# Kernel tuning notes

Hardware: AMD Instinct MI355X
Metric: run time of the kernel (lower is better)

## Reference

```python
import jax, jax.numpy as jnp
import numpy as np

# Group structure (matches init_kwargs)
SIZES = np.array([16]*16 + [32]*32 + [64]*16)          # teacher_embedding_sizes_list
CHOICES = np.array([4]*16 + [8]*32 + [16]*16)          # max_choice_per_embedding
IN_DIM = int(SIZES.sum())                               # 2304
OUT_DIM = int(CHOICES.sum())                            # 576
W_TOTAL = int((SIZES * CHOICES).sum())                  # 25600
BATCH = 16384


def setup_inputs() -> dict:
    key = jax.random.key(0)
    k1, k2 = jax.random.split(key)
    x = jax.random.normal(k1, (BATCH, IN_DIM), dtype=jnp.float32)
    # TruncatedNormal(stddev=0.15) approximated with scaled normal
    weight = jax.random.normal(k2, (W_TOTAL, 1), dtype=jnp.float32) * 0.15
    bias = jnp.zeros((OUT_DIM,), dtype=jnp.float32)
    return {"x": x, "weight": weight, "bias": bias}


def reference(x, weight, bias):
    # Block-diagonal grouped GEMM: per-group slice of x times per-group weight
    # block reshaped to [size_i, choice_i], concatenated along features + bias.
    w_flat = weight[:, 0]
    outs = []
    w_idx = 0
    t_idx = 0
    for size, choice in zip(SIZES.tolist(), CHOICES.tolist()):
        x_slice = x[:, t_idx:t_idx + size]                       # [B, size]
        w_block = w_flat[w_idx:w_idx + size * choice].reshape(size, choice)
        outs.append(x_slice @ w_block)                           # [B, choice]
        w_idx += size * choice
        t_idx += size
    return jnp.concatenate(outs, axis=1) + bias
```

## Files before the change

### kernel.cpp

```cpp
#include <hip/hip_runtime.h>


#define BATCH   16384
#define IN_DIM  2304
#define OUT_DIM 576
#define CHUNKS  36
#define XS_LDW  68

__global__ __launch_bounds__(256) void fused_block_mm(
    const float* __restrict__ x, const float* __restrict__ w,
    const float* __restrict__ bias, float* __restrict__ out)
{
    __shared__ float xs[64 * XS_LDW];
    __shared__ float wd[64 * 16];

    const int tid = threadIdx.x;
    const int bx  = blockIdx.x;
    const int cj  = bx % CHUNKS;
    const int rt  = bx / CHUNKS;
    const int row_base = rt * 64;

    if (cj < 4) {
        const int wbase = cj * 256;
        #pragma unroll
        for (int i = 0; i < 4; ++i) {
            const int e = tid + i * 256, k = e >> 4, c = e & 15, b = k >> 4;
            wd[e] = ((c >> 2) == b)
                  ? w[wbase + b * 64 + ((k & 15) << 2) + (c & 3)] : 0.0f;
        }
    } else if (cj < 20) {
        const int wbase = 1024 + (cj - 4) * 512;
        #pragma unroll
        for (int i = 0; i < 4; ++i) {
            const int e = tid + i * 256, k = e >> 4, c = e & 15, b = k >> 5;
            wd[e] = ((c >> 3) == b)
                  ? w[wbase + b * 256 + ((k & 31) << 3) + (c & 7)] : 0.0f;
        }
    } else {
        const int wbase = 9216 + (cj - 20) * 1024;
        #pragma unroll
        for (int i = 0; i < 4; ++i) {
            const int e = tid + i * 256;
            wd[e] = w[wbase + e];
        }
    }

    const float* __restrict__ xsrc = x + (size_t)row_base * IN_DIM + cj * 64;
    #pragma unroll
    for (int i = 0; i < 4; ++i) {
        const int f = tid + i * 256, r = f >> 4, c = (f & 15) << 2;
        const float4 v = *reinterpret_cast<const float4*>(
            xsrc + (size_t)r * IN_DIM + c);
        *reinterpret_cast<float4*>(&xs[r * XS_LDW + c]) = v;
    }
    __syncthreads();

    const int wv   = __builtin_amdgcn_readfirstlane(tid >> 6);
    const int lane = tid & 63;
    const int ocol = cj * 16 + (wv << 2);

    float4 acc = make_float4(bias[ocol], bias[ocol + 1],
                             bias[ocol + 2], bias[ocol + 3]);

    const int xb = lane * XS_LDW;
    const int wb = wv << 2;
    #pragma unroll
    for (int k4 = 0; k4 < 16; ++k4) {
        const float4 xv = *reinterpret_cast<const float4*>(&xs[xb + (k4 << 2)]);
        const float4 w0 = *reinterpret_cast<const float4*>(&wd[(k4*4+0)*16 + wb]);
        const float4 w1 = *reinterpret_cast<const float4*>(&wd[(k4*4+1)*16 + wb]);
        const float4 w2 = *reinterpret_cast<const float4*>(&wd[(k4*4+2)*16 + wb]);
        const float4 w3 = *reinterpret_cast<const float4*>(&wd[(k4*4+3)*16 + wb]);
        acc.x += xv.x*w0.x + xv.y*w1.x + xv.z*w2.x + xv.w*w3.x;
        acc.y += xv.x*w0.y + xv.y*w1.y + xv.z*w2.y + xv.w*w3.y;
        acc.z += xv.x*w0.z + xv.y*w1.z + xv.z*w2.z + xv.w*w3.z;
        acc.w += xv.x*w0.w + xv.y*w1.w + xv.z*w2.w + xv.w*w3.w;
    }

    float* __restrict__ op = out + (size_t)(row_base + lane) * OUT_DIM + ocol;
    *reinterpret_cast<float4*>(op) = acc;
}

extern "C" void kernel_launch(void* const* d_in, const int* in_sizes, int n_in,
                              void* d_out, int out_size, void* d_ws, size_t ws_size,
                              hipStream_t stream) {
    const float* x    = (const float*)d_in[0];
    const float* w    = (const float*)d_in[1];
    const float* bias = (const float*)d_in[2];
    float* out        = (float*)d_out;

    const int row_tiles = BATCH / 64;
    fused_block_mm<<<dim3(CHUNKS * row_tiles), 256, 0, stream>>>(
        x, w, bias, out);
}
```

Baseline: 228.6 us.

## Give each wave its own 64-row x tile and all 16 output columns

Each block now has 128 threads (two waves) and covers 128 rows. Each wave loads its own 64-row slice of x into a private shared-memory buffer, and each lane computes all 16 output columns of its row. Before, four waves each computed 4 columns over the same 64 rows. This reuses each x element across 16 outputs in registers, needs no barrier after the x load, and halves the grid size, while the shared weight tile is loaded once per 128 rows. The cost is more accumulator registers per thread and fewer threads per block, so there is less parallelism to hide memory latency on what is a bandwidth-bound kernel.

```diff
diff --git a/kernel.cpp b/kernel.cpp
--- a/kernel.cpp
+++ b/kernel.cpp
@@ -7,78 +7,89 @@
 #define CHUNKS  36
 #define XS_LDW  68
 
-__global__ __launch_bounds__(256) void fused_block_mm(
+__global__ __launch_bounds__(128) void fused_block_mm(
     const float* __restrict__ x, const float* __restrict__ w,
     const float* __restrict__ bias, float* __restrict__ out)
 {
-    __shared__ float xs[64 * XS_LDW];
     __shared__ float wd[64 * 16];
+    __shared__ float xs[2][64 * XS_LDW];
 
     const int tid = threadIdx.x;
     const int bx  = blockIdx.x;
     const int cj  = bx % CHUNKS;
     const int rt  = bx / CHUNKS;
-    const int row_base = rt * 64;
 
     if (cj < 4) {
         const int wbase = cj * 256;
         #pragma unroll
-        for (int i = 0; i < 4; ++i) {
-            const int e = tid + i * 256, k = e >> 4, c = e & 15, b = k >> 4;
+        for (int i = 0; i < 8; ++i) {
+            const int e = tid + i * 128, k = e >> 4, c = e & 15, b = k >> 4;
             wd[e] = ((c >> 2) == b)
                   ? w[wbase + b * 64 + ((k & 15) << 2) + (c & 3)] : 0.0f;
         }
     } else if (cj < 20) {
         const int wbase = 1024 + (cj - 4) * 512;
         #pragma unroll
-        for (int i = 0; i < 4; ++i) {
-            const int e = tid + i * 256, k = e >> 4, c = e & 15, b = k >> 5;
+        for (int i = 0; i < 8; ++i) {
+            const int e = tid + i * 128, k = e >> 4, c = e & 15, b = k >> 5;
             wd[e] = ((c >> 3) == b)
                   ? w[wbase + b * 256 + ((k & 31) << 3) + (c & 7)] : 0.0f;
         }
     } else {
         const int wbase = 9216 + (cj - 20) * 1024;
         #pragma unroll
-        for (int i = 0; i < 4; ++i) {
-            const int e = tid + i * 256;
+        for (int i = 0; i < 8; ++i) {
+            const int e = tid + i * 128;
             wd[e] = w[wbase + e];
         }
     }
+    __syncthreads();
 
-    const float* __restrict__ xsrc = x + (size_t)row_base * IN_DIM + cj * 64;
+    const int wv   = tid >> 6;
+    const int lane = tid & 63;
+    float* __restrict__ xsw = xs[wv];
+    const int row0 = rt * 128 + wv * 64;
+
+    const float* __restrict__ xsrc = x + (size_t)row0 * IN_DIM + cj * 64;
     #pragma unroll
-    for (int i = 0; i < 4; ++i) {
-        const int f = tid + i * 256, r = f >> 4, c = (f & 15) << 2;
+    for (int i = 0; i < 16; ++i) {
+        const int f = (i << 6) + lane;
+        const int r = f >> 4, c = (f & 15) << 2;
         const float4 v = *reinterpret_cast<const float4*>(
             xsrc + (size_t)r * IN_DIM + c);
-        *reinterpret_cast<float4*>(&xs[r * XS_LDW + c]) = v;
+        *reinterpret_cast<float4*>(&xsw[r * XS_LDW + c]) = v;
     }
-    __syncthreads();
 
-    const int wv   = __builtin_amdgcn_readfirstlane(tid >> 6);
-    const int lane = tid & 63;
-    const int ocol = cj * 16 + (wv << 2);
-
-    float4 acc = make_float4(bias[ocol], bias[ocol + 1],
-                             bias[ocol + 2], bias[ocol + 3]);
+    const int ocol = cj * 16;
+    float4 a0 = *reinterpret_cast<const float4*>(&bias[ocol + 0]);
+    float4 a1 = *reinterpret_cast<const float4*>(&bias[ocol + 4]);
+    float4 a2 = *reinterpret_cast<const float4*>(&bias[ocol + 8]);
+    float4 a3 = *reinterpret_cast<const float4*>(&bias[ocol + 12]);
 
     const int xb = lane * XS_LDW;
-    const int wb = wv << 2;
     #pragma unroll
     for (int k4 = 0; k4 < 16; ++k4) {
-        const float4 xv = *reinterpret_cast<const float4*>(&xs[xb + (k4 << 2)]);
-        const float4 w0 = *reinterpret_cast<const float4*>(&wd[(k4*4+0)*16 + wb]);
-        const float4 w1 = *reinterpret_cast<const float4*>(&wd[(k4*4+1)*16 + wb]);
-        const float4 w2 = *reinterpret_cast<const float4*>(&wd[(k4*4+2)*16 + wb]);
-        const float4 w3 = *reinterpret_cast<const float4*>(&wd[(k4*4+3)*16 + wb]);
-        acc.x += xv.x*w0.x + xv.y*w1.x + xv.z*w2.x + xv.w*w3.x;
-        acc.y += xv.x*w0.y + xv.y*w1.y + xv.z*w2.y + xv.w*w3.y;
-        acc.z += xv.x*w0.z + xv.y*w1.z + xv.z*w2.z + xv.w*w3.z;
-        acc.w += xv.x*w0.w + xv.y*w1.w + xv.z*w2.w + xv.w*w3.w;
+        const float4 xv = *reinterpret_cast<const float4*>(&xsw[xb + (k4 << 2)]);
+        #pragma unroll
+        for (int j = 0; j < 4; ++j) {
+            const float xj = j == 0 ? xv.x : j == 1 ? xv.y : j == 2 ? xv.z : xv.w;
+            const float* __restrict__ wr = &wd[((k4 << 2) + j) << 4];
+            const float4 w0 = *reinterpret_cast<const float4*>(wr + 0);
+            const float4 w1 = *reinterpret_cast<const float4*>(wr + 4);
+            const float4 w2 = *reinterpret_cast<const float4*>(wr + 8);
+            const float4 w3 = *reinterpret_cast<const float4*>(wr + 12);
+            a0.x += xj * w0.x; a0.y += xj * w0.y; a0.z += xj * w0.z; a0.w += xj * w0.w;
+            a1.x += xj * w1.x; a1.y += xj * w1.y; a1.z += xj * w1.z; a1.w += xj * w1.w;
+            a2.x += xj * w2.x; a2.y += xj * w2.y; a2.z += xj * w2.z; a2.w += xj * w2.w;
+            a3.x += xj * w3.x; a3.y += xj * w3.y; a3.z += xj * w3.z; a3.w += xj * w3.w;
+        }
     }
 
-    float* __restrict__ op = out + (size_t)(row_base + lane) * OUT_DIM + ocol;
-    *reinterpret_cast<float4*>(op) = acc;
+    float* __restrict__ op = out + (size_t)(row0 + lane) * OUT_DIM + ocol;
+    reinterpret_cast<float4*>(op)[0] = a0;
+    reinterpret_cast<float4*>(op)[1] = a1;
+    reinterpret_cast<float4*>(op)[2] = a2;
+    reinterpret_cast<float4*>(op)[3] = a3;
 }
 
 extern "C" void kernel_launch(void* const* d_in, const int* in_sizes, int n_in,
@@ -89,7 +100,5 @@
     const float* bias = (const float*)d_in[2];
     float* out        = (float*)d_out;
 
-    const int row_tiles = BATCH / 64;
-    fused_block_mm<<<dim3(CHUNKS * row_tiles), 256, 0, stream>>>(
-        x, w, bias, out);
+    fused_block_mm<<<dim3(CHUNKS * 128), 128, 0, stream>>>(x, w, bias, out);
 }
```

After: 234.7 us. +2.7%, slower.

## Process 256 rows per block with register-prefetched K-slab pipeline

Applied to the files above, without the earlier changes.

Each block now handles 256 rows instead of 64. The block streams x in four 16-column K slabs through a small shared buffer, prefetching the next slab into registers while it computes on the current one. This cuts the number of blocks and the per-block weight staging overhead by a factor of four, and each thread now keeps four row accumulators. The trade-offs are fewer blocks in flight (2304 total), more syncthreads per block, and higher register pressure, partly addressed by a launch-bounds occupancy hint.

```diff
diff --git a/kernel.cpp b/kernel.cpp
--- a/kernel.cpp
+++ b/kernel.cpp
@@ -5,20 +5,29 @@
 #define IN_DIM  2304
 #define OUT_DIM 576
 #define CHUNKS  36
-#define XS_LDW  68
+#define XS_LDW  20
 
-__global__ __launch_bounds__(256) void fused_block_mm(
+__global__ __launch_bounds__(256, 4) void fused_block_mm(
     const float* __restrict__ x, const float* __restrict__ w,
     const float* __restrict__ bias, float* __restrict__ out)
 {
-    __shared__ float xs[64 * XS_LDW];
+    __shared__ float xs[256 * XS_LDW];
     __shared__ float wd[64 * 16];
 
-    const int tid = threadIdx.x;
-    const int bx  = blockIdx.x;
-    const int cj  = bx % CHUNKS;
-    const int rt  = bx / CHUNKS;
-    const int row_base = rt * 64;
+    const int tid  = threadIdx.x;
+    const int bx   = blockIdx.x;
+    const int cj   = bx % CHUNKS;
+    const int rt   = bx / CHUNKS;
+    const int row0 = rt * 256;
+
+    const float* __restrict__ xsrc = x + (size_t)row0 * IN_DIM + cj * 64;
+    const int lr = tid >> 2;
+    const int lk = (tid & 3) << 2;
+    float4 pf[4];
+    #pragma unroll
+    for (int i = 0; i < 4; ++i)
+        pf[i] = *reinterpret_cast<const float4*>(
+            xsrc + (size_t)(lr + 64 * i) * IN_DIM + lk);
 
     if (cj < 4) {
         const int wbase = cj * 256;
@@ -44,41 +53,53 @@
             wd[e] = w[wbase + e];
         }
     }
-
-    const float* __restrict__ xsrc = x + (size_t)row_base * IN_DIM + cj * 64;
-    #pragma unroll
-    for (int i = 0; i < 4; ++i) {
-        const int f = tid + i * 256, r = f >> 4, c = (f & 15) << 2;
-        const float4 v = *reinterpret_cast<const float4*>(
-            xsrc + (size_t)r * IN_DIM + c);
-        *reinterpret_cast<float4*>(&xs[r * XS_LDW + c]) = v;
-    }
     __syncthreads();
 
     const int wv   = __builtin_amdgcn_readfirstlane(tid >> 6);
     const int lane = tid & 63;
     const int ocol = cj * 16 + (wv << 2);
 
-    float4 acc = make_float4(bias[ocol], bias[ocol + 1],
-                             bias[ocol + 2], bias[ocol + 3]);
+    const float4 bv = *reinterpret_cast<const float4*>(bias + ocol);
+    float4 acc[4] = {bv, bv, bv, bv};
 
-    const int xb = lane * XS_LDW;
-    const int wb = wv << 2;
     #pragma unroll
-    for (int k4 = 0; k4 < 16; ++k4) {
-        const float4 xv = *reinterpret_cast<const float4*>(&xs[xb + (k4 << 2)]);
-        const float4 w0 = *reinterpret_cast<const float4*>(&wd[(k4*4+0)*16 + wb]);
-        const float4 w1 = *reinterpret_cast<const float4*>(&wd[(k4*4+1)*16 + wb]);
-        const float4 w2 = *reinterpret_cast<const float4*>(&wd[(k4*4+2)*16 + wb]);
-        const float4 w3 = *reinterpret_cast<const float4*>(&wd[(k4*4+3)*16 + wb]);
-        acc.x += xv.x*w0.x + xv.y*w1.x + xv.z*w2.x + xv.w*w3.x;
-        acc.y += xv.x*w0.y + xv.y*w1.y + xv.z*w2.y + xv.w*w3.y;
-        acc.z += xv.x*w0.z + xv.y*w1.z + xv.z*w2.z + xv.w*w3.z;
-        acc.w += xv.x*w0.w + xv.y*w1.w + xv.z*w2.w + xv.w*w3.w;
+    for (int s = 0; s < 4; ++s) {
+        #pragma unroll
+        for (int i = 0; i < 4; ++i)
+            *reinterpret_cast<float4*>(&xs[(lr + 64 * i) * XS_LDW + lk]) = pf[i];
+        __syncthreads();
+
+        if (s < 3) {
+            #pragma unroll
+            for (int i = 0; i < 4; ++i)
+                pf[i] = *reinterpret_cast<const float4*>(
+                    xsrc + (size_t)(lr + 64 * i) * IN_DIM + (s + 1) * 16 + lk);
+        }
+
+        #pragma unroll
+        for (int k4 = 0; k4 < 4; ++k4) {
+            const int kb = (s << 4) + (k4 << 2);
+            const float4 w0 = *reinterpret_cast<const float4*>(&wd[(kb+0)*16 + (wv<<2)]);
+            const float4 w1 = *reinterpret_cast<const float4*>(&wd[(kb+1)*16 + (wv<<2)]);
+            const float4 w2 = *reinterpret_cast<const float4*>(&wd[(kb+2)*16 + (wv<<2)]);
+            const float4 w3 = *reinterpret_cast<const float4*>(&wd[(kb+3)*16 + (wv<<2)]);
+            #pragma unroll
+            for (int j = 0; j < 4; ++j) {
+                const float4 xv = *reinterpret_cast<const float4*>(
+                    &xs[(lane + 64 * j) * XS_LDW + (k4 << 2)]);
+                acc[j].x += xv.x*w0.x + xv.y*w1.x + xv.z*w2.x + xv.w*w3.x;
+                acc[j].y += xv.x*w0.y + xv.y*w1.y + xv.z*w2.y + xv.w*w3.y;
+                acc[j].z += xv.x*w0.z + xv.y*w1.z + xv.z*w2.z + xv.w*w3.z;
+                acc[j].w += xv.x*w0.w + xv.y*w1.w + xv.z*w2.w + xv.w*w3.w;
+            }
+        }
+        if (s < 3) __syncthreads();
     }
 
-    float* __restrict__ op = out + (size_t)(row_base + lane) * OUT_DIM + ocol;
-    *reinterpret_cast<float4*>(op) = acc;
+    #pragma unroll
+    for (int j = 0; j < 4; ++j)
+        *reinterpret_cast<float4*>(
+            out + (size_t)(row0 + lane + 64 * j) * OUT_DIM + ocol) = acc[j];
 }
 
 extern "C" void kernel_launch(void* const* d_in, const int* in_sizes, int n_in,
@@ -89,7 +110,5 @@
     const float* bias = (const float*)d_in[2];
     float* out        = (float*)d_out;
 
-    const int row_tiles = BATCH / 64;
-    fused_block_mm<<<dim3(CHUNKS * row_tiles), 256, 0, stream>>>(
-        x, w, bias, out);
+    fused_block_mm<<<dim3(CHUNKS * 64), 256, 0, stream>>>(x, w, bias, out);
 }
```

Result: slower. 636.0 us (+178.2%).
